# Optimization experiments

Measured on AMD Instinct MI355X. Metric: run time of the kernel, lower is better.

## Reference

```python
import jax, jax.numpy as jnp
import numpy as np

B, SEQ, DIM = 1, 720, 2048
N_HEADS, HEAD_DIM = 16, 128
CACHE_SIZE = 11520
SINK_TOKENS = 720
CURRENT_START = 11520
FRAME_SEQLEN = 720
EPS = 1e-6


def _rmsnorm(x, w, eps=EPS):
    # WanRMSNorm: x * rsqrt(mean(x^2) + eps) * weight
    return x * jax.lax.rsqrt(jnp.mean(x * x, axis=-1, keepdims=True) + eps) * w


def _rope(x, cos, sin):
    # x: [b, s, n, d]; pairs are consecutive (reshape(..., d//2, 2)) as in causal_rope_apply
    b, s, n, d = x.shape
    xp = x.reshape(b, s, n, d // 2, 2)
    xr, xi = xp[..., 0], xp[..., 1]
    c = cos[None, :, None, :]
    sn = sin[None, :, None, :]
    out = jnp.stack([xr * c - xi * sn, xr * sn + xi * c], axis=-1)
    return out.reshape(b, s, n, d)


def _make_freqs():
    # precompute_freqs_i_t_only: head_dim//2 = 64 complex freqs; first 22 temporal
    # (rope_t_params with dim = 128 - 4*(128//6) = 44 -> 22 freqs), h/w parts use
    # table row 0 -> angle 0 (identity).
    f, h, w = 1, 20, 36
    t0 = CURRENT_START // FRAME_SEQLEN  # 16
    c = HEAD_DIM // 2
    dim_t = 44
    inv = 1.0 / (10000.0 ** (np.arange(0, dim_t, 2, dtype=np.float64) / dim_t))  # [22]
    ang_t = np.outer(np.arange(f, dtype=np.float64) + t0, inv)  # [f, 22]
    ang = np.zeros((f, h, w, c), dtype=np.float64)
    ang[..., : inv.shape[0]] = ang_t[:, None, None, :]
    ang = ang.reshape(f * h * w, c)
    return np.cos(ang).astype(np.float32), np.sin(ang).astype(np.float32)


def setup_inputs() -> dict:
    key = jax.random.key(0)
    ks = jax.random.split(key, 8)
    w_scale = 0.02
    cos, sin = _make_freqs()
    return {
        "x": jax.random.normal(ks[0], (B, SEQ, DIM), jnp.float32),
        "q_w": jax.random.normal(ks[1], (DIM, DIM), jnp.float32) * w_scale,
        "q_b": jnp.zeros((DIM,), jnp.float32),
        "k_w": jax.random.normal(ks[2], (DIM, DIM), jnp.float32) * w_scale,
        "k_b": jnp.zeros((DIM,), jnp.float32),
        "v_w": jax.random.normal(ks[3], (DIM, DIM), jnp.float32) * w_scale,
        "v_b": jnp.zeros((DIM,), jnp.float32),
        "o_w": jax.random.normal(ks[4], (DIM, DIM), jnp.float32) * w_scale,
        "o_b": jnp.zeros((DIM,), jnp.float32),
        "norm_q_w": jnp.ones((DIM,), jnp.float32),
        "norm_k_w": jnp.ones((DIM,), jnp.float32),
        "cache_k": jax.random.normal(ks[5], (B, CACHE_SIZE, N_HEADS, HEAD_DIM), jnp.float32),
        "cache_v": jax.random.normal(ks[6], (B, CACHE_SIZE, N_HEADS, HEAD_DIM), jnp.float32),
        "freqs_cos": jnp.asarray(cos),
        "freqs_sin": jnp.asarray(sin),
        "current_start": CURRENT_START,
        "frame_seqlen": FRAME_SEQLEN,
        "sink_tokens": SINK_TOKENS,
    }


def reference(x, q_w, q_b, k_w, k_b, v_w, v_b, o_w, o_b, norm_q_w, norm_k_w,
              cache_k, cache_v, freqs_cos, freqs_sin,
              current_start, frame_seqlen, sink_tokens):
    b, s, _ = x.shape
    n, d = cache_k.shape[2], cache_k.shape[3]
    # qkv projections with qk RMSNorm
    q = _rmsnorm(x @ q_w.T + q_b, norm_q_w).reshape(b, s, n, d)
    k = _rmsnorm(x @ k_w.T + k_b, norm_k_w).reshape(b, s, n, d)
    v = (x @ v_w.T + v_b).reshape(b, s, n, d)
    # RoPE on new q/k (causal_rope_apply with precomputed freqs_i)
    rq = _rope(q, freqs_cos, freqs_sin)
    rk = _rope(k, freqs_cos, freqs_sin)
    # rolling KV-cache write (contiguous case: local_end > local_start)
    cache_size = cache_k.shape[1]
    rolling = cache_size - sink_tokens
    local_start = (current_start - sink_tokens) % rolling + sink_tokens
    k_all = jax.lax.dynamic_update_slice(cache_k, rk, (0, local_start, 0, 0))
    v_all = jax.lax.dynamic_update_slice(cache_v, v, (0, local_start, 0, 0))
    # full-cache attention branch (cache_size == sink + max_attention, current_end >= cache_size)
    scale = d ** -0.5
    scores = jnp.einsum('bqnd,bknd->bnqk', rq, k_all) * scale  # [b, n, s, cache]
    probs = jax.nn.softmax(scores, axis=-1)
    out = jnp.einsum('bnqk,bknd->bqnd', probs, v_all).reshape(b, s, n * d)
    return out @ o_w.T + o_b
```

## Files before the change

### kernel.cpp

```cpp
#include <hip/hip_runtime.h>

#define SEQ 720
#define DIM 2048
#define NH 16
#define HD 128
#define CACHE 11520
#define KSP 8
#define LOG2E 1.4426950408889634f
#define SM_SCALE 0.08838834764831845f
#define CSCL (SM_SCALE * LOG2E)

typedef unsigned short u16;
typedef unsigned int u32;
typedef __bf16 bf8_t __attribute__((ext_vector_type(8)));
typedef float f4 __attribute__((ext_vector_type(4)));

__device__ __forceinline__ float bf2f(u16 v) {
    union { u32 u; float f; } t; t.u = ((u32)v) << 16; return t.f;
}
__device__ __forceinline__ u16 f2bf(float f) {
    union { float f; u32 u; } t; t.f = f;
    u32 u = t.u;
    return (u16)((u + 0x7fffu + ((u >> 16) & 1u)) >> 16);
}
__device__ __forceinline__ u16 f2bf_fast(float f) {
    __bf16 h = (__bf16)f;
    return __builtin_bit_cast(u16, h);
}
__device__ __forceinline__ bf8_t ld_bf8(const u16* p) {
    const u16* pa = (const u16*)__builtin_assume_aligned(p, 16);
    bf8_t r;
    __builtin_memcpy(&r, pa, 16);
    return r;
}
__device__ __forceinline__ uint4 ld_u4g(const u16* p) {
    uint4 r;
    __builtin_memcpy(&r, (const u16*)__builtin_assume_aligned(p, 16), 16);
    return r;
}
__device__ __forceinline__ void st_u4l(u16* p, uint4 v) {
    __builtin_memcpy((u16*)__builtin_assume_aligned(p, 16), &v, 16);
}
__device__ __forceinline__ void st8(u16* p, const u16* v) {
    __builtin_memcpy((u16*)__builtin_assume_aligned(p, 16), v, 16);
}
__device__ __forceinline__ void ld8_cvt(const void* base, size_t off, int f32, u16* dst) {
    if (f32) {
        const float* p = (const float*)base + off;
        float v[8];
        __builtin_memcpy(v, (const float*)__builtin_assume_aligned(p, 16), 32);
        #pragma unroll
        for (int i = 0; i < 8; i++) dst[i] = f2bf(v[i]);
    } else {
        const u16* p = (const u16*)base + off;
        __builtin_memcpy(dst, (const u16*)__builtin_assume_aligned(p, 16), 16);
    }
}
__device__ __forceinline__ float ld1(const void* base, size_t off, int f32) {
    return f32 ? ((const float*)base)[off] : bf2f(((const u16*)base)[off]);
}
__device__ __forceinline__ int ls_from(const int* cs_p, const int* sink_p) {
    const int cs = cs_p[0], sink = sink_p[0];
    const int rolling = CACHE - sink;
    int ls = (cs - sink) % rolling + sink;
    if (ls > CACHE - SEQ) ls = CACHE - SEQ;
    return ls;
}

__device__ __forceinline__ void cp16_lds(u16* lds, const u16* g) {
    __builtin_amdgcn_global_load_lds(
        (const __attribute__((address_space(1))) void*)g,
        (__attribute__((address_space(3))) void*)lds,
        16, 0, 0);
}

__global__ __launch_bounds__(256) void detect_kernel(const void* probe, int* flag) {
    __shared__ int cnt[256];
    const int tid = threadIdx.x;
    const u16* p = (const u16*)probe;
    int bad = 0;
    for (int i = tid; i < 4096; i += 256) {
        int e = (p[i] >> 7) & 0xFF;
        bad += (e < 0x60 || e > 0x90) ? 1 : 0;
    }
    cnt[tid] = bad;
    __syncthreads();
    if (tid == 0) {
        int s = 0;
        for (int i = 0; i < 256; i++) s += cnt[i];
        flag[0] = (s > 256) ? 1 : 0;
    }
}

__global__ __launch_bounds__(256) void zero_kernel(float* p, int n) {
    int i = blockIdx.x * 256 + threadIdx.x;
    if (i < n) p[i] = 0.f;
}

__global__ __launch_bounds__(256) void cvt3_kernel(
    const void* __restrict__ s0, const void* __restrict__ s1, const void* __restrict__ s2,
    u16* __restrict__ d0, u16* __restrict__ d1, u16* __restrict__ d2,
    int n, const int* __restrict__ dflag)
{
    const int f32 = dflag[0];
    const int z = blockIdx.y;
    const void* s = (z == 0) ? s0 : (z == 1) ? s1 : s2;
    u16* d = (z == 0) ? d0 : (z == 1) ? d1 : d2;
    const int idx = (blockIdx.x * 256 + threadIdx.x) * 8;
    if (idx < n) {
        u16 t[8];
        ld8_cvt(s, idx, f32, t);
        st8(d + idx, t);
    }
}

__device__ __forceinline__ void gemm2_body(const u16* __restrict__ A,
                                           const u16* __restrict__ W,
                                           const u16* __restrict__ bias,
                                           void* __restrict__ C, int cF32, int M)
{
    __shared__ __align__(16) u16 As[64 * 64];
    __shared__ __align__(16) u16 Bs[128 * 64];
    const int tid = threadIdx.x;
    const int wv = tid >> 6, lane = tid & 63, quad = lane >> 4, l16 = lane & 15;
    const int n0 = blockIdx.x * 128, m0 = blockIdx.y * 64;
    const int wr = (wv & 1) * 32, wc = (wv >> 1) * 64;

    f4 acc[2][4];
    #pragma unroll
    for (int i = 0; i < 2; i++)
        #pragma unroll
        for (int j = 0; j < 4; j++)
            acc[i][j] = f4{0.f, 0.f, 0.f, 0.f};

    const int srow = tid >> 3, scb = tid & 7;

    for (int kb = 0; kb < DIM / 64; kb++) {
        const int k0 = kb * 64;
        uint4 av[2], bv[4];
        #pragma unroll
        for (int i = 0; i < 2; i++) {
            const int row = srow + 32 * i;
            int gm = m0 + row; if (gm >= M) gm = M - 1;
            av[i] = ld_u4g(A + (size_t)gm * DIM + k0 + scb * 8);
        }
        #pragma unroll
        for (int i = 0; i < 4; i++) {
            const int row = srow + 32 * i;
            bv[i] = ld_u4g(W + (size_t)(n0 + row) * DIM + k0 + scb * 8);
        }
        __syncthreads();
        #pragma unroll
        for (int i = 0; i < 2; i++) {
            const int row = srow + 32 * i;
            st_u4l(&As[row * 64 + ((scb ^ (row & 7)) * 8)], av[i]);
        }
        #pragma unroll
        for (int i = 0; i < 4; i++) {
            const int row = srow + 32 * i;
            st_u4l(&Bs[row * 64 + ((scb ^ (row & 7)) * 8)], bv[i]);
        }
        __syncthreads();
        #pragma unroll
        for (int s = 0; s < 2; s++) {
            bf8_t af[2], bfr[4];
            #pragma unroll
            for (int i = 0; i < 2; i++) {
                const int m = wr + i * 16 + l16;
                af[i]  = ld_bf8(&As[m * 64 + (((s * 4 + quad) ^ (m & 7)) * 8)]);
            }
            #pragma unroll
            for (int i = 0; i < 4; i++) {
                const int n = wc + i * 16 + l16;
                bfr[i] = ld_bf8(&Bs[n * 64 + (((s * 4 + quad) ^ (n & 7)) * 8)]);
            }
            #pragma unroll
            for (int mi = 0; mi < 2; mi++)
                #pragma unroll
                for (int nj = 0; nj < 4; nj++)
                    acc[mi][nj] = __builtin_amdgcn_mfma_f32_16x16x32_bf16(af[mi], bfr[nj], acc[mi][nj], 0, 0, 0);
        }
    }

    #pragma unroll
    for (int mi = 0; mi < 2; mi++) {
        const int rowb = m0 + wr + mi * 16 + quad * 4;
        #pragma unroll
        for (int r = 0; r < 4; r++) {
            if (rowb + r < M) {
                #pragma unroll
                for (int nj = 0; nj < 4; nj++) {
                    const int col = n0 + wc + nj * 16 + l16;
                    float v = acc[mi][nj][r] + bf2f(bias[col]);
                    if (cF32) ((float*)C)[(size_t)(rowb + r) * DIM + col] = v;
                    else      ((u16*)C)[(size_t)(rowb + r) * DIM + col] = f2bf(v);
                }
            }
        }
    }
}

__global__ __launch_bounds__(256) void gemm2_qkv_kernel(
    const u16* __restrict__ X,
    const u16* __restrict__ w0, const u16* __restrict__ w1, const u16* __restrict__ w2,
    const u16* __restrict__ b0, const u16* __restrict__ b1, const u16* __restrict__ b2,
    u16* __restrict__ o0, u16* __restrict__ o1, u16* __restrict__ o2, int M)
{
    const int z = blockIdx.z;
    const u16* W = (z == 0) ? w0 : (z == 1) ? w1 : w2;
    const u16* B = (z == 0) ? b0 : (z == 1) ? b1 : b2;
    u16* O = (z == 0) ? o0 : (z == 1) ? o1 : o2;
    gemm2_body(X, W, B, O, 0, M);
}

__global__ __launch_bounds__(256) void gemm2_o_kernel(
    const u16* __restrict__ X, const u16* __restrict__ W,
    const u16* __restrict__ B, void* __restrict__ O,
    const int* __restrict__ dflag, int M)
{
    gemm2_body(X, W, B, O, dflag[0], M);
}

__global__ __launch_bounds__(256) void normrope_kernel(
    u16* __restrict__ qbuf, u16* __restrict__ kbuf,
    const void* __restrict__ nqw, const void* __restrict__ nkw,
    const void* __restrict__ fcos, const void* __restrict__ fsin,
    const int* __restrict__ dflag)
{
    const int f32 = dflag[0];
    const int row = blockIdx.x, z = blockIdx.y;
    const int tid = threadIdx.x, lane = tid & 63, wvi = tid >> 6;
    u16* buf = ((z == 0) ? qbuf : kbuf) + (size_t)row * DIM + tid * 8;
    u16 in[8];
    __builtin_memcpy(in, (const u16*)__builtin_assume_aligned(buf, 16), 16);
    float x[8];
    #pragma unroll
    for (int i = 0; i < 8; i++) x[i] = bf2f(in[i]);
    float ss = 0.f;
    #pragma unroll
    for (int i = 0; i < 8; i++) ss += x[i] * x[i];
    ss += __shfl_xor(ss, 32); ss += __shfl_xor(ss, 16); ss += __shfl_xor(ss, 8);
    ss += __shfl_xor(ss, 4);  ss += __shfl_xor(ss, 2);  ss += __shfl_xor(ss, 1);
    __shared__ float red[4];
    if (lane == 0) red[wvi] = ss;
    __syncthreads();
    const float rinv = rsqrtf((red[0] + red[1] + red[2] + red[3]) * (1.0f / DIM) + 1e-6f);
    const void* wn = (z == 0) ? nqw : nkw;
    float y[8];
    #pragma unroll
    for (int i = 0; i < 8; i++) y[i] = x[i] * rinv * ld1(wn, tid * 8 + i, f32);
    const int dd = (tid * 8) & (HD - 1);
    const int cb = row * 64 + (dd >> 1);
    u16 outv[8];
    #pragma unroll
    for (int p = 0; p < 4; p++) {
        float cv = ld1(fcos, cb + p, f32), sv = ld1(fsin, cb + p, f32);
        float xr = y[2 * p], xi = y[2 * p + 1];
        outv[2 * p]     = f2bf(xr * cv - xi * sv);
        outv[2 * p + 1] = f2bf(xr * sv + xi * cv);
    }
    __builtin_memcpy((u16*)__builtin_assume_aligned(buf, 16), outv, 16);
}

__global__ __launch_bounds__(256) void cvtk_kernel(
    const void* __restrict__ cache_k, const u16* __restrict__ kr,
    u16* __restrict__ Kb, const int* __restrict__ cs_p,
    const int* __restrict__ sink_p, const int* __restrict__ dflag)
{
    const int f32 = dflag[0];
    const int kt = blockIdx.x, h = blockIdx.y, tid = threadIdx.x;
    const int ls = ls_from(cs_p, sink_p);
    #pragma unroll
    for (int i = 0; i < 8; i++) {
        const int idx = i * 2048 + tid * 8;
        const int key = kt * 128 + (idx >> 7);
        const int d0 = idx & 127;
        u16 tmp[8];
        if (key >= ls && key < ls + SEQ)
            ld8_cvt(kr, (size_t)(key - ls) * DIM + h * HD + d0, 0, tmp);
        else
            ld8_cvt(cache_k, (size_t)key * DIM + h * HD + d0, f32, tmp);
        st8(&Kb[((size_t)h * CACHE + key) * HD + d0], tmp);
    }
}

__device__ __forceinline__ int swz(int ky, int cb) {
    return (cb ^ (ky >> 3) ^ ((ky & 7) << 1)) & 15;
}

__global__ __launch_bounds__(256) void cvtv_kernel(
    const void* __restrict__ cache_v, const u16* __restrict__ vr,
    u16* __restrict__ Vt, const int* __restrict__ cs_p,
    const int* __restrict__ sink_p, const int* __restrict__ dflag)
{
    __shared__ __align__(16) u16 Vtile[128 * 128];
    const int f32 = dflag[0];
    const int kt = blockIdx.x, h = blockIdx.y, tid = threadIdx.x;
    const int ls = ls_from(cs_p, sink_p);
    #pragma unroll
    for (int i = 0; i < 8; i++) {
        const int idx = i * 2048 + tid * 8;
        const int ky = idx >> 7;
        const int d0 = idx & 127;
        const int key = kt * 128 + ky;
        u16 tmp[8];
        if (key >= ls && key < ls + SEQ)
            ld8_cvt(vr, (size_t)(key - ls) * DIM + h * HD + d0, 0, tmp);
        else
            ld8_cvt(cache_v, (size_t)key * DIM + h * HD + d0, f32, tmp);
        st8(&Vtile[ky * 128 + swz(ky, d0 >> 3) * 8], tmp);
    }
    __syncthreads();
    #pragma unroll
    for (int i = 0; i < 8; i++) {
        const int oidx = i * 2048 + tid * 8;
        const int d = oidx >> 7;
        const int k8 = oidx & 127;
        u16 o[8];
        #pragma unroll
        for (int j = 0; j < 8; j++) {
            const int ky = k8 + j;
            o[j] = Vtile[ky * 128 + swz(ky, d >> 3) * 8 + (d & 7)];
        }
        st8(&Vt[((size_t)h * HD + d) * CACHE + kt * 128 + k8], o);
    }
}

__global__ __launch_bounds__(256, 3) void attn2_kernel(
    const u16* __restrict__ qr, const u16* __restrict__ Kb, const u16* __restrict__ Vt,
    float* __restrict__ pO, float* __restrict__ pL)
{
    __shared__ __align__(16) u16 Klds[2][32 * 128];
    __shared__ __align__(16) u16 Vlds[3][128 * 32];
    __shared__ __align__(16) u16 Ps[4][32 * 40];
    const int tid = threadIdx.x;
    const int wvi = tid >> 6, lane = tid & 63, quad = lane >> 4, l16 = lane & 15;
    const int kc = blockIdx.x, qb = blockIdx.y, h = blockIdx.z;
    const int q0 = qb * 128 + wvi * 32;
    const int kch = CACHE / KSP;
    const int ktiles = kch / 32;

    bf8_t aQ[2][4];
    #pragma unroll
    for (int mi = 0; mi < 2; mi++) {
        int qrow = q0 + mi * 16 + l16; if (qrow >= SEQ) qrow = SEQ - 1;
        const u16* qp = qr + (size_t)qrow * DIM + h * HD + quad * 8;
        #pragma unroll
        for (int dc = 0; dc < 4; dc++) aQ[mi][dc] = ld_bf8(qp + dc * 32);
    }

    f4 O[2][8];
    float lsum[2][4];
    #pragma unroll
    for (int mi = 0; mi < 2; mi++) {
        #pragma unroll
        for (int dc = 0; dc < 8; dc++) O[mi][dc] = f4{0.f, 0.f, 0.f, 0.f};
        #pragma unroll
        for (int r = 0; r < 4; r++) lsum[mi][r] = 0.f;
    }

    const u16* kbase = Kb + ((size_t)h * CACHE + (size_t)kc * kch) * HD;
    const u16* vbase = Vt + (size_t)h * HD * CACHE + (size_t)kc * kch;

    const int s0 = tid, s1 = tid + 256;
    const int koff0 = (s0 >> 4) * HD + (((s0 & 15) ^ ((s0 >> 4) & 15)) * 8);
    const int koff1 = (s1 >> 4) * HD + (((s1 & 15) ^ ((s1 >> 4) & 15)) * 8);
    const size_t voff0 = (size_t)(s0 >> 2) * CACHE
                       + (((s0 & 3) ^ ((s0 >> 2) & 3) ^ ((s0 >> 4) & 3)) * 8);
    const size_t voff1 = (size_t)(s1 >> 2) * CACHE
                       + (((s1 & 3) ^ ((s1 >> 2) & 3) ^ ((s1 >> 4) & 3)) * 8);

    auto stageK = [&](int t, int b) {
        const u16* kp = kbase + (size_t)t * 32 * HD;
        cp16_lds(&Klds[b][wvi * 512], kp + koff0);
        cp16_lds(&Klds[b][2048 + wvi * 512], kp + koff1);
    };
    auto stageV = [&](int t, int b) {
        const u16* vp = vbase + t * 32;
        cp16_lds(&Vlds[b][wvi * 512], vp + voff0);
        cp16_lds(&Vlds[b][2048 + wvi * 512], vp + voff1);
    };
    auto qkt = [&](int b, f4 sc[2][2]) {
        bf8_t kf[8];
        #pragma unroll
        for (int dc = 0; dc < 4; dc++) {
            const int g8 = ((quad + 4 * dc) ^ l16) * 8;
            kf[dc]     = ld_bf8(&Klds[b][l16 * HD + g8]);
            kf[4 + dc] = ld_bf8(&Klds[b][(16 + l16) * HD + g8]);
        }
        #pragma unroll
        for (int mi = 0; mi < 2; mi++) { sc[mi][0] = f4{0.f,0.f,0.f,0.f}; sc[mi][1] = f4{0.f,0.f,0.f,0.f}; }
        #pragma unroll
        for (int dc = 0; dc < 4; dc++) {
            #pragma unroll
            for (int mi = 0; mi < 2; mi++) {
                sc[mi][0] = __builtin_amdgcn_mfma_f32_16x16x32_bf16(aQ[mi][dc], kf[dc],     sc[mi][0], 0, 0, 0);
                sc[mi][1] = __builtin_amdgcn_mfma_f32_16x16x32_bf16(aQ[mi][dc], kf[4 + dc], sc[mi][1], 0, 0, 0);
            }
        }
    };
    auto smax = [&](const f4 sc[2][2]) {
        #pragma unroll
        for (int mi = 0; mi < 2; mi++) {
            #pragma unroll
            for (int r = 0; r < 4; r++) {
                float p0 = exp2f(sc[mi][0][r] * CSCL);
                float p1 = exp2f(sc[mi][1][r] * CSCL);
                lsum[mi][r] += p0 + p1;
                const int prow = mi * 16 + quad * 4 + r;
                Ps[wvi][prow * 40 + l16]      = f2bf_fast(p0);
                Ps[wvi][prow * 40 + 16 + l16] = f2bf_fast(p1);
            }
        }
    };
    const int vq8 = (quad ^ (l16 & 3) ^ (l16 >> 2)) * 8;
    auto pv = [&](bf8_t ap0, bf8_t ap1, int vb) {
        bf8_t vf[8];
        #pragma unroll
        for (int dc = 0; dc < 8; dc++)
            vf[dc] = ld_bf8(&Vlds[vb][(dc * 16 + l16) * 32 + vq8]);
        #pragma unroll
        for (int dc = 0; dc < 8; dc++) {
            O[0][dc] = __builtin_amdgcn_mfma_f32_16x16x32_bf16(ap0, vf[dc], O[0][dc], 0, 0, 0);
            O[1][dc] = __builtin_amdgcn_mfma_f32_16x16x32_bf16(ap1, vf[dc], O[1][dc], 0, 0, 0);
        }
    };

    stageK(0, 0);
    stageV(0, 0);
    __syncthreads();

    {
        stageK(1, 1);
        stageV(1, 1);
        f4 sc[2][2];
        qkt(0, sc);
        smax(sc);
        __syncthreads();
    }

    int vr = 0, vs = 2;
    for (int t = 1; t < ktiles; t++) {
        const int kb = t & 1;
        if (t + 1 < ktiles) {
            stageK(t + 1, kb ^ 1);
            stageV(t + 1, vs);
        }
        f4 sc[2][2];
        qkt(kb, sc);
        bf8_t ap0 = ld_bf8(&Ps[wvi][l16 * 40 + quad * 8]);
        bf8_t ap1 = ld_bf8(&Ps[wvi][(16 + l16) * 40 + quad * 8]);
        smax(sc);
        pv(ap0, ap1, vr);
        __syncthreads();
        vr = (vr == 2) ? 0 : vr + 1;
        vs = (vs == 2) ? 0 : vs + 1;
    }

    {
        bf8_t ap0 = ld_bf8(&Ps[wvi][l16 * 40 + quad * 8]);
        bf8_t ap1 = ld_bf8(&Ps[wvi][(16 + l16) * 40 + quad * 8]);
        pv(ap0, ap1, vr);
    }

    #pragma unroll
    for (int mi = 0; mi < 2; mi++)
        #pragma unroll
        for (int r = 0; r < 4; r++) {
            float s = lsum[mi][r];
            s += __shfl_xor(s, 1); s += __shfl_xor(s, 2);
            s += __shfl_xor(s, 4); s += __shfl_xor(s, 8);
            lsum[mi][r] = s;
        }
    #pragma unroll
    for (int mi = 0; mi < 2; mi++) {
        #pragma unroll
        for (int r = 0; r < 4; r++) {
            const int q = q0 + mi * 16 + quad * 4 + r;
            if (q < SEQ) {
                const size_t rb = (size_t)(h * SEQ + q);
                const size_t pb = (rb * KSP + kc) * HD;
                #pragma unroll
                for (int dc = 0; dc < 8; dc++)
                    pO[pb + dc * 16 + l16] = O[mi][dc][r];
                if (l16 == 0) atomicAdd(&pL[rb], lsum[mi][r]);
            }
        }
    }
}

__global__ __launch_bounds__(128) void combine2_kernel(
    const float* __restrict__ pO, const float* __restrict__ pL,
    u16* __restrict__ attn)
{
    const int q = blockIdx.x, h = blockIdx.y, d = threadIdx.x;
    const size_t rb = (size_t)(h * SEQ + q);
    float num = 0.f;
    for (int s = 0; s < KSP; s++)
        num += pO[(rb * KSP + s) * HD + d];
    attn[(size_t)q * DIM + h * HD + d] = f2bf(num / pL[rb]);
}

extern "C" void kernel_launch(void* const* d_in, const int* in_sizes, int n_in,
                              void* d_out, int out_size, void* d_ws, size_t ws_size,
                              hipStream_t stream)
{
    const void* x    = d_in[0];
    const void* q_w  = d_in[1];
    const void* q_b  = d_in[2];
    const void* k_w  = d_in[3];
    const void* k_b  = d_in[4];
    const void* v_w  = d_in[5];
    const void* v_b  = d_in[6];
    const void* o_w  = d_in[7];
    const void* o_b  = d_in[8];
    const void* nqw  = d_in[9];
    const void* nkw  = d_in[10];
    const void* cK   = d_in[11];
    const void* cV   = d_in[12];
    const void* fcos = d_in[13];
    const void* fsin = d_in[14];
    const int* cs_p   = (const int*)d_in[15];
    const int* sink_p = (const int*)d_in[17];

    char* ws = (char*)d_ws;
    const size_t SZB  = (size_t)SEQ * DIM * 2;
    const size_t KBsz = (size_t)NH * CACHE * HD * 2;
    const size_t PO1  = (size_t)NH * SEQ * HD * 4;

    int*  dflag = (int*)ws;
    u16*  q_l   = (u16*)(ws + 256);
    u16*  k_l   = (u16*)(ws + 256 + SZB);
    u16*  v_l   = (u16*)(ws + 256 + 2 * SZB);
    u16*  attn  = (u16*)(ws + 256 + 3 * SZB);
    char* pbase = ws + 256 + 4 * SZB;
    u16*   Kb = (u16*)pbase;
    u16*   Vt = (u16*)(pbase + KBsz);
    float* pO = (float*)(pbase + 2 * KBsz);
    float* pL = (float*)(pbase + 2 * KBsz + (size_t)KSP * PO1);

    u16* Wq = (u16*)pO;
    u16* Wk = Wq + (size_t)DIM * DIM;
    u16* Wv = Wk + (size_t)DIM * DIM;
    u16* x_bf = Wv + (size_t)DIM * DIM;
    u16* bq = x_bf + (size_t)SEQ * DIM;
    u16* bk = bq + DIM;
    u16* bv = bk + DIM;
    u16* Wo = (u16*)pO;
    u16* bo = Wo + (size_t)DIM * DIM;

    dim3 blk(256);
    detect_kernel<<<1, blk, 0, stream>>>(q_w, dflag);

    cvt3_kernel<<<dim3(DIM * DIM / 2048, 3), blk, 0, stream>>>(
        q_w, k_w, v_w, Wq, Wk, Wv, DIM * DIM, dflag);
    cvt3_kernel<<<dim3(SEQ * DIM / 2048, 1), blk, 0, stream>>>(
        x, x, x, x_bf, x_bf, x_bf, SEQ * DIM, dflag);
    cvt3_kernel<<<dim3(1, 3), blk, 0, stream>>>(
        q_b, k_b, v_b, bq, bk, bv, DIM, dflag);
    gemm2_qkv_kernel<<<dim3(16, 12, 3), blk, 0, stream>>>(
        x_bf, Wq, Wk, Wv, bq, bk, bv, q_l, k_l, v_l, SEQ);
    normrope_kernel<<<dim3(SEQ, 2), blk, 0, stream>>>(
        q_l, k_l, nqw, nkw, fcos, fsin, dflag);

    cvtk_kernel<<<dim3(CACHE / 128, NH), blk, 0, stream>>>(cK, k_l, Kb, cs_p, sink_p, dflag);
    cvtv_kernel<<<dim3(CACHE / 128, NH), blk, 0, stream>>>(cV, v_l, Vt, cs_p, sink_p, dflag);
    {
        int nL = NH * SEQ;
        zero_kernel<<<(nL + 255) / 256, blk, 0, stream>>>(pL, nL);
    }
    attn2_kernel<<<dim3(KSP, 6, NH), blk, 0, stream>>>(q_l, Kb, Vt, pO, pL);
    combine2_kernel<<<dim3(SEQ, NH), dim3(128), 0, stream>>>(pO, pL, attn);

    cvt3_kernel<<<dim3(DIM * DIM / 2048, 1), blk, 0, stream>>>(
        o_w, o_w, o_w, Wo, Wo, Wo, DIM * DIM, dflag);
    cvt3_kernel<<<dim3(1, 1), blk, 0, stream>>>(
        o_b, o_b, o_b, bo, bo, bo, DIM, dflag);
    gemm2_o_kernel<<<dim3(16, 12, 1), blk, 0, stream>>>(
        attn, Wo, bo, d_out, dflag, SEQ);
}
```

Before: 500.5 us.

## Fuse fp32-to-bf16 conversion into GEMM loads and drop atomic row-sum zeroing

Removes the standalone conversion kernels for the projection weights, input activations and biases, and converts fp32 to bf16 while loading GEMM tiles instead. Attention per-split row sums are written to a scratch array reused from the V buffer and summed in the combine kernel, so the zeroing kernel and the atomics go away. This saves a full read/write pass over the weights and several launches. In exchange, the GEMM tile loads now move twice the bytes when inputs are fp32.

```diff
diff --git a/kernel.cpp b/kernel.cpp
--- a/kernel.cpp
+++ b/kernel.cpp
@@ -33,14 +33,6 @@
     __builtin_memcpy(&r, pa, 16);
     return r;
 }
-__device__ __forceinline__ uint4 ld_u4g(const u16* p) {
-    uint4 r;
-    __builtin_memcpy(&r, (const u16*)__builtin_assume_aligned(p, 16), 16);
-    return r;
-}
-__device__ __forceinline__ void st_u4l(u16* p, uint4 v) {
-    __builtin_memcpy((u16*)__builtin_assume_aligned(p, 16), &v, 16);
-}
 __device__ __forceinline__ void st8(u16* p, const u16* v) {
     __builtin_memcpy((u16*)__builtin_assume_aligned(p, 16), v, 16);
 }
@@ -92,31 +84,9 @@
     }
 }
 
-__global__ __launch_bounds__(256) void zero_kernel(float* p, int n) {
-    int i = blockIdx.x * 256 + threadIdx.x;
-    if (i < n) p[i] = 0.f;
-}
-
-__global__ __launch_bounds__(256) void cvt3_kernel(
-    const void* __restrict__ s0, const void* __restrict__ s1, const void* __restrict__ s2,
-    u16* __restrict__ d0, u16* __restrict__ d1, u16* __restrict__ d2,
-    int n, const int* __restrict__ dflag)
-{
-    const int f32 = dflag[0];
-    const int z = blockIdx.y;
-    const void* s = (z == 0) ? s0 : (z == 1) ? s1 : s2;
-    u16* d = (z == 0) ? d0 : (z == 1) ? d1 : d2;
-    const int idx = (blockIdx.x * 256 + threadIdx.x) * 8;
-    if (idx < n) {
-        u16 t[8];
-        ld8_cvt(s, idx, f32, t);
-        st8(d + idx, t);
-    }
-}
-
-__device__ __forceinline__ void gemm2_body(const u16* __restrict__ A,
-                                           const u16* __restrict__ W,
-                                           const u16* __restrict__ bias,
+__device__ __forceinline__ void gemm2_body(const void* __restrict__ A, int aF32,
+                                           const void* __restrict__ W,
+                                           const void* __restrict__ bias, int wF32,
                                            void* __restrict__ C, int cF32, int M)
 {
     __shared__ __align__(16) u16 As[64 * 64];
@@ -137,28 +107,28 @@
 
     for (int kb = 0; kb < DIM / 64; kb++) {
         const int k0 = kb * 64;
-        uint4 av[2], bv[4];
+        u16 avt[2][8], bvt[4][8];
         #pragma unroll
         for (int i = 0; i < 2; i++) {
             const int row = srow + 32 * i;
             int gm = m0 + row; if (gm >= M) gm = M - 1;
-            av[i] = ld_u4g(A + (size_t)gm * DIM + k0 + scb * 8);
+            ld8_cvt(A, (size_t)gm * DIM + k0 + scb * 8, aF32, avt[i]);
         }
         #pragma unroll
         for (int i = 0; i < 4; i++) {
             const int row = srow + 32 * i;
-            bv[i] = ld_u4g(W + (size_t)(n0 + row) * DIM + k0 + scb * 8);
+            ld8_cvt(W, (size_t)(n0 + row) * DIM + k0 + scb * 8, wF32, bvt[i]);
         }
         __syncthreads();
         #pragma unroll
         for (int i = 0; i < 2; i++) {
             const int row = srow + 32 * i;
-            st_u4l(&As[row * 64 + ((scb ^ (row & 7)) * 8)], av[i]);
+            st8(&As[row * 64 + ((scb ^ (row & 7)) * 8)], avt[i]);
         }
         #pragma unroll
         for (int i = 0; i < 4; i++) {
             const int row = srow + 32 * i;
-            st_u4l(&Bs[row * 64 + ((scb ^ (row & 7)) * 8)], bv[i]);
+            st8(&Bs[row * 64 + ((scb ^ (row & 7)) * 8)], bvt[i]);
         }
         __syncthreads();
         #pragma unroll
@@ -191,7 +161,7 @@
                 #pragma unroll
                 for (int nj = 0; nj < 4; nj++) {
                     const int col = n0 + wc + nj * 16 + l16;
-                    float v = acc[mi][nj][r] + bf2f(bias[col]);
+                    float v = acc[mi][nj][r] + ld1(bias, col, wF32);
                     if (cF32) ((float*)C)[(size_t)(rowb + r) * DIM + col] = v;
                     else      ((u16*)C)[(size_t)(rowb + r) * DIM + col] = f2bf(v);
                 }
@@ -201,24 +171,27 @@
 }
 
 __global__ __launch_bounds__(256) void gemm2_qkv_kernel(
-    const u16* __restrict__ X,
-    const u16* __restrict__ w0, const u16* __restrict__ w1, const u16* __restrict__ w2,
-    const u16* __restrict__ b0, const u16* __restrict__ b1, const u16* __restrict__ b2,
-    u16* __restrict__ o0, u16* __restrict__ o1, u16* __restrict__ o2, int M)
+    const void* __restrict__ X,
+    const void* __restrict__ w0, const void* __restrict__ w1, const void* __restrict__ w2,
+    const void* __restrict__ b0, const void* __restrict__ b1, const void* __restrict__ b2,
+    u16* __restrict__ o0, u16* __restrict__ o1, u16* __restrict__ o2,
+    const int* __restrict__ dflag, int M)
 {
     const int z = blockIdx.z;
-    const u16* W = (z == 0) ? w0 : (z == 1) ? w1 : w2;
-    const u16* B = (z == 0) ? b0 : (z == 1) ? b1 : b2;
+    const void* W = (z == 0) ? w0 : (z == 1) ? w1 : w2;
+    const void* B = (z == 0) ? b0 : (z == 1) ? b1 : b2;
     u16* O = (z == 0) ? o0 : (z == 1) ? o1 : o2;
-    gemm2_body(X, W, B, O, 0, M);
+    const int f32 = dflag[0];
+    gemm2_body(X, f32, W, B, f32, O, 0, M);
 }
 
 __global__ __launch_bounds__(256) void gemm2_o_kernel(
-    const u16* __restrict__ X, const u16* __restrict__ W,
-    const u16* __restrict__ B, void* __restrict__ O,
+    const u16* __restrict__ X, const void* __restrict__ W,
+    const void* __restrict__ B, void* __restrict__ O,
     const int* __restrict__ dflag, int M)
 {
-    gemm2_body(X, W, B, O, dflag[0], M);
+    const int f32 = dflag[0];
+    gemm2_body(X, 0, W, B, f32, O, f32, M);
 }
 
 __global__ __launch_bounds__(256) void normrope_kernel(
@@ -328,7 +301,7 @@
 
 __global__ __launch_bounds__(256, 3) void attn2_kernel(
     const u16* __restrict__ qr, const u16* __restrict__ Kb, const u16* __restrict__ Vt,
-    float* __restrict__ pO, float* __restrict__ pL)
+    float* __restrict__ pO, float* __restrict__ pLp)
 {
     __shared__ __align__(16) u16 Klds[2][32 * 128];
     __shared__ __align__(16) u16 Vlds[3][128 * 32];
@@ -483,22 +456,25 @@
                 #pragma unroll
                 for (int dc = 0; dc < 8; dc++)
                     pO[pb + dc * 16 + l16] = O[mi][dc][r];
-                if (l16 == 0) atomicAdd(&pL[rb], lsum[mi][r]);
+                if (l16 == 0) pLp[rb * KSP + kc] = lsum[mi][r];
             }
         }
     }
 }
 
 __global__ __launch_bounds__(128) void combine2_kernel(
-    const float* __restrict__ pO, const float* __restrict__ pL,
+    const float* __restrict__ pO, const float* __restrict__ pLp,
     u16* __restrict__ attn)
 {
     const int q = blockIdx.x, h = blockIdx.y, d = threadIdx.x;
     const size_t rb = (size_t)(h * SEQ + q);
-    float num = 0.f;
-    for (int s = 0; s < KSP; s++)
+    float num = 0.f, den = 0.f;
+    #pragma unroll
+    for (int s = 0; s < KSP; s++) {
         num += pO[(rb * KSP + s) * HD + d];
-    attn[(size_t)q * DIM + h * HD + d] = f2bf(num / pL[rb]);
+        den += pLp[rb * KSP + s];
+    }
+    attn[(size_t)q * DIM + h * HD + d] = f2bf(num / den);
 }
 
 extern "C" void kernel_launch(void* const* d_in, const int* in_sizes, int n_in,
@@ -537,45 +513,21 @@
     u16*   Kb = (u16*)pbase;
     u16*   Vt = (u16*)(pbase + KBsz);
     float* pO = (float*)(pbase + 2 * KBsz);
-    float* pL = (float*)(pbase + 2 * KBsz + (size_t)KSP * PO1);
-
-    u16* Wq = (u16*)pO;
-    u16* Wk = Wq + (size_t)DIM * DIM;
-    u16* Wv = Wk + (size_t)DIM * DIM;
-    u16* x_bf = Wv + (size_t)DIM * DIM;
-    u16* bq = x_bf + (size_t)SEQ * DIM;
-    u16* bk = bq + DIM;
-    u16* bv = bk + DIM;
-    u16* Wo = (u16*)pO;
-    u16* bo = Wo + (size_t)DIM * DIM;
+    float* pLp = (float*)v_l;
 
     dim3 blk(256);
     detect_kernel<<<1, blk, 0, stream>>>(q_w, dflag);
 
-    cvt3_kernel<<<dim3(DIM * DIM / 2048, 3), blk, 0, stream>>>(
-        q_w, k_w, v_w, Wq, Wk, Wv, DIM * DIM, dflag);
-    cvt3_kernel<<<dim3(SEQ * DIM / 2048, 1), blk, 0, stream>>>(
-        x, x, x, x_bf, x_bf, x_bf, SEQ * DIM, dflag);
-    cvt3_kernel<<<dim3(1, 3), blk, 0, stream>>>(
-        q_b, k_b, v_b, bq, bk, bv, DIM, dflag);
     gemm2_qkv_kernel<<<dim3(16, 12, 3), blk, 0, stream>>>(
-        x_bf, Wq, Wk, Wv, bq, bk, bv, q_l, k_l, v_l, SEQ);
+        x, q_w, k_w, v_w, q_b, k_b, v_b, q_l, k_l, v_l, dflag, SEQ);
     normrope_kernel<<<dim3(SEQ, 2), blk, 0, stream>>>(
         q_l, k_l, nqw, nkw, fcos, fsin, dflag);
 
     cvtk_kernel<<<dim3(CACHE / 128, NH), blk, 0, stream>>>(cK, k_l, Kb, cs_p, sink_p, dflag);
     cvtv_kernel<<<dim3(CACHE / 128, NH), blk, 0, stream>>>(cV, v_l, Vt, cs_p, sink_p, dflag);
-    {
-        int nL = NH * SEQ;
-        zero_kernel<<<(nL + 255) / 256, blk, 0, stream>>>(pL, nL);
-    }
-    attn2_kernel<<<dim3(KSP, 6, NH), blk, 0, stream>>>(q_l, Kb, Vt, pO, pL);
-    combine2_kernel<<<dim3(SEQ, NH), dim3(128), 0, stream>>>(pO, pL, attn);
-
-    cvt3_kernel<<<dim3(DIM * DIM / 2048, 1), blk, 0, stream>>>(
-        o_w, o_w, o_w, Wo, Wo, Wo, DIM * DIM, dflag);
-    cvt3_kernel<<<dim3(1, 1), blk, 0, stream>>>(
-        o_b, o_b, o_b, bo, bo, bo, DIM, dflag);
+    attn2_kernel<<<dim3(KSP, 6, NH), blk, 0, stream>>>(q_l, Kb, Vt, pO, pLp);
+    combine2_kernel<<<dim3(SEQ, NH), dim3(128), 0, stream>>>(pO, pLp, attn);
+
     gemm2_o_kernel<<<dim3(16, 12, 1), blk, 0, stream>>>(
-        attn, Wo, bo, d_out, dflag, SEQ);
-}
+        attn, o_w, o_b, d_out, dflag, SEQ);
+}
```

Result: slower. 608.0 us (+21.5%).
